# Optimization experiments

Measured on AMD Instinct MI355X. Metric: run time of the kernel, lower is better.

## Reference

```python
import jax, jax.numpy as jnp
import numpy as np

THRESHOLD = 0.3
NUM_VERTICES = 6890  # SMPL mesh
B, V, H, W = 8, 4, 512, 512


def setup_inputs() -> dict:
    key = jax.random.key(0)
    k1, k2, k3 = jax.random.split(key, 3)
    seg_maps = jax.random.uniform(k1, (B, V, H, W), dtype=jnp.float32)
    # indices in [-1, NUM_VERTICES): -1 marks background pixels (filtered as out-of-range)
    pixel_to_vertex_map = jax.random.randint(k2, (V, H, W, 3), -1, NUM_VERTICES, dtype=jnp.int32)
    bary_coord_map = jax.random.uniform(k3, (V, H, W, 3), dtype=jnp.float32)
    return {"seg_maps": seg_maps, "pixel_to_vertex_map": pixel_to_vertex_map,
            "bary_coord_map": bary_coord_map}


def reference(seg_maps, pixel_to_vertex_map, bary_coord_map):
    dtype = seg_maps.dtype
    verts = pixel_to_vertex_map                                  # [V,H,W,3]
    # a pixel contributes only if ALL 3 of its vertex ids are in range
    valid = jnp.all((verts >= 0) & (verts < NUM_VERTICES), axis=-1)  # [V,H,W]
    mask = seg_maps > THRESHOLD                                   # [B,V,H,W]
    eff = (mask & valid[None]).astype(dtype)                      # [B,V,H,W]
    w = bary_coord_map[None] * eff[..., None]                     # [B,V,H,W,3]
    ones = jnp.broadcast_to(eff[..., None], w.shape)              # per-coord count contrib
    # invalid indices were zeroed-out in weights; clamp them to 0 for a safe scatter
    idx = jnp.where(valid[..., None], verts, 0).reshape(-1)       # [V*H*W*3]
    wf = w.reshape(seg_maps.shape[0], -1)
    cf = ones.reshape(seg_maps.shape[0], -1)
    scatter = jax.vmap(lambda v: jnp.zeros((NUM_VERTICES,), dtype).at[idx].add(v))
    pred = scatter(wf)                                            # [B, NUM_VERTICES]
    count = scatter(cf)
    safe = jnp.where(count > 0, count, jnp.ones((), dtype))
    pred = jnp.where(count > 0, pred / safe, pred)
    return (pred > THRESHOLD).astype(dtype)
```

## Files before the change

kernel.cpp:

```cpp
#include <hip/hip_runtime.h>
#include <hip/hip_bf16.h>
#include <stdint.h>

#define NUM_VERTICES 6890
#define THRESHOLD 0.3f
#define B_DIM 8
#define V_DIM 4
#define H_DIM 512
#define W_DIM 512
#define TOTAL_PIX (V_DIM * H_DIM * W_DIM)
#define CHUNKS 64
#define BLOCK_THREADS 1024

#define FRAC 262144.0f
#define CNT_ONE (1u << 25)
#define SUM_MASK ((1u << 25) - 1)

__device__ __forceinline__ uint32_t pack_w(float w) {
    return CNT_ONE + (uint32_t)(w * FRAC + 0.5f);
}
__device__ __forceinline__ void lds_uadd(uint32_t* p, uint32_t v) {
    __hip_atomic_fetch_add(p, v, __ATOMIC_RELAXED, __HIP_MEMORY_SCOPE_WORKGROUP);
}

__global__ __launch_bounds__(BLOCK_THREADS)
void hc3d_accum_pair_kernel(const float* __restrict__ seg,
                            const int* __restrict__ verts,
                            const float* __restrict__ bary,
                            uint32_t* __restrict__ partial) {
    __shared__ uint32_t s_hist0[NUM_VERTICES];
    __shared__ uint32_t s_hist1[NUM_VERTICES];

    const int pr = blockIdx.y;
    const int c  = blockIdx.x;
    for (int i = threadIdx.x; i < NUM_VERTICES; i += BLOCK_THREADS) {
        s_hist0[i] = 0u;
        s_hist1[i] = 0u;
    }
    __syncthreads();

    const int groupsPerChunk = (TOTAL_PIX / CHUNKS) / 4;
    const int gStart = c * groupsPerChunk;

    const float4* __restrict__ seg0 =
        reinterpret_cast<const float4*>(seg + (size_t)(2 * pr) * TOTAL_PIX);
    const float4* __restrict__ seg1 =
        reinterpret_cast<const float4*>(seg + (size_t)(2 * pr + 1) * TOTAL_PIX);
    const int4* __restrict__ verts4  = reinterpret_cast<const int4*>(verts);
    const float4* __restrict__ bary4 = reinterpret_cast<const float4*>(bary);

    #pragma unroll 2
    for (int g = gStart + threadIdx.x; g < gStart + groupsPerChunk;
         g += BLOCK_THREADS) {
        const float4 sA = seg0[g];
        const float4 sB = seg1[g];
        const int4   va = verts4[3 * (size_t)g + 0];
        const int4   vb = verts4[3 * (size_t)g + 1];
        const int4   vc = verts4[3 * (size_t)g + 2];
        const float4 wa = bary4[3 * (size_t)g + 0];
        const float4 wb = bary4[3 * (size_t)g + 1];
        const float4 wc = bary4[3 * (size_t)g + 2];

        {
            const bool valid = ((unsigned)va.x < NUM_VERTICES) &
                               ((unsigned)va.y < NUM_VERTICES) &
                               ((unsigned)va.z < NUM_VERTICES);
            const uint32_t p0 = pack_w(wa.x), p1 = pack_w(wa.y), p2 = pack_w(wa.z);
            if (valid & (sA.x > THRESHOLD)) {
                lds_uadd(&s_hist0[va.x], p0);
                lds_uadd(&s_hist0[va.y], p1);
                lds_uadd(&s_hist0[va.z], p2);
            }
            if (valid & (sB.x > THRESHOLD)) {
                lds_uadd(&s_hist1[va.x], p0);
                lds_uadd(&s_hist1[va.y], p1);
                lds_uadd(&s_hist1[va.z], p2);
            }
        }
        {
            const bool valid = ((unsigned)va.w < NUM_VERTICES) &
                               ((unsigned)vb.x < NUM_VERTICES) &
                               ((unsigned)vb.y < NUM_VERTICES);
            const uint32_t p0 = pack_w(wa.w), p1 = pack_w(wb.x), p2 = pack_w(wb.y);
            if (valid & (sA.y > THRESHOLD)) {
                lds_uadd(&s_hist0[va.w], p0);
                lds_uadd(&s_hist0[vb.x], p1);
                lds_uadd(&s_hist0[vb.y], p2);
            }
            if (valid & (sB.y > THRESHOLD)) {
                lds_uadd(&s_hist1[va.w], p0);
                lds_uadd(&s_hist1[vb.x], p1);
                lds_uadd(&s_hist1[vb.y], p2);
            }
        }
        {
            const bool valid = ((unsigned)vb.z < NUM_VERTICES) &
                               ((unsigned)vb.w < NUM_VERTICES) &
                               ((unsigned)vc.x < NUM_VERTICES);
            const uint32_t p0 = pack_w(wb.z), p1 = pack_w(wb.w), p2 = pack_w(wc.x);
            if (valid & (sA.z > THRESHOLD)) {
                lds_uadd(&s_hist0[vb.z], p0);
                lds_uadd(&s_hist0[vb.w], p1);
                lds_uadd(&s_hist0[vc.x], p2);
            }
            if (valid & (sB.z > THRESHOLD)) {
                lds_uadd(&s_hist1[vb.z], p0);
                lds_uadd(&s_hist1[vb.w], p1);
                lds_uadd(&s_hist1[vc.x], p2);
            }
        }
        {
            const bool valid = ((unsigned)vc.y < NUM_VERTICES) &
                               ((unsigned)vc.z < NUM_VERTICES) &
                               ((unsigned)vc.w < NUM_VERTICES);
            const uint32_t p0 = pack_w(wc.y), p1 = pack_w(wc.z), p2 = pack_w(wc.w);
            if (valid & (sA.w > THRESHOLD)) {
                lds_uadd(&s_hist0[vc.y], p0);
                lds_uadd(&s_hist0[vc.z], p1);
                lds_uadd(&s_hist0[vc.w], p2);
            }
            if (valid & (sB.w > THRESHOLD)) {
                lds_uadd(&s_hist1[vc.y], p0);
                lds_uadd(&s_hist1[vc.z], p1);
                lds_uadd(&s_hist1[vc.w], p2);
            }
        }
    }
    __syncthreads();

    uint32_t* __restrict__ pb0 =
        partial + ((size_t)(c * 4 + pr) * 2 + 0) * NUM_VERTICES;
    uint32_t* __restrict__ pb1 =
        partial + ((size_t)(c * 4 + pr) * 2 + 1) * NUM_VERTICES;
    for (int i = threadIdx.x; i < NUM_VERTICES; i += BLOCK_THREADS) {
        pb0[i] = s_hist0[i];
        pb1[i] = s_hist1[i];
    }
}

__global__ __launch_bounds__(256)
void hc3d_finalize_sum_kernel(const uint32_t* __restrict__ partial,
                              float* __restrict__ out) {
    const int idx = blockIdx.x * 256 + threadIdx.x;
    if (idx < B_DIM * NUM_VERTICES) {
        const int b = idx / NUM_VERTICES;
        const int v = idx - b * NUM_VERTICES;
        const size_t slot = (size_t)b * NUM_VERTICES + v;
        uint32_t cnt = 0u, sumf = 0u;
        #pragma unroll
        for (int c = 0; c < CHUNKS; ++c) {
            const uint32_t p =
                partial[(size_t)c * (B_DIM * NUM_VERTICES) + slot];
            cnt  += p >> 25;
            sumf += p & SUM_MASK;
        }
        const float sum = (float)sumf * (1.0f / FRAC);
        const float val = (cnt > 0u) ? (sum / (float)cnt) : sum;
        out[idx] = (val > THRESHOLD) ? 1.0f : 0.0f;
    }
}

__global__ __launch_bounds__(BLOCK_THREADS)
void hc3d_accum_at_kernel(const float* __restrict__ seg,
                          const int* __restrict__ verts,
                          const float* __restrict__ bary,
                          uint32_t* __restrict__ acc) {
    const int b = blockIdx.y;
    const int c = blockIdx.x;
    const int groupsPerChunk = (TOTAL_PIX / CHUNKS) / 4;
    const int gStart = c * groupsPerChunk;
    const float4* __restrict__ seg4  =
        reinterpret_cast<const float4*>(seg + (size_t)b * TOTAL_PIX);
    const int4* __restrict__ verts4  = reinterpret_cast<const int4*>(verts);
    const float4* __restrict__ bary4 = reinterpret_cast<const float4*>(bary);
    uint32_t* predf = acc + (size_t)b * NUM_VERTICES;
    uint32_t* cnt   = acc + (size_t)(B_DIM + b) * NUM_VERTICES;

    for (int g = gStart + threadIdx.x; g < gStart + groupsPerChunk;
         g += BLOCK_THREADS) {
        const float4 s4 = seg4[g];
        const int4   va = verts4[3 * (size_t)g + 0];
        const int4   vb = verts4[3 * (size_t)g + 1];
        const int4   vc = verts4[3 * (size_t)g + 2];
        const float4 wa = bary4[3 * (size_t)g + 0];
        const float4 wb = bary4[3 * (size_t)g + 1];
        const float4 wc = bary4[3 * (size_t)g + 2];
        const float  ss[4] = {s4.x, s4.y, s4.z, s4.w};
        const int    vv[12] = {va.x,va.y,va.z, va.w,vb.x,vb.y,
                               vb.z,vb.w,vc.x, vc.y,vc.z,vc.w};
        const float  ww[12] = {wa.x,wa.y,wa.z, wa.w,wb.x,wb.y,
                               wb.z,wb.w,wc.x, wc.y,wc.z,wc.w};
        #pragma unroll
        for (int p = 0; p < 4; ++p) {
            const bool ok = (ss[p] > THRESHOLD) &
                            ((unsigned)vv[3*p+0] < NUM_VERTICES) &
                            ((unsigned)vv[3*p+1] < NUM_VERTICES) &
                            ((unsigned)vv[3*p+2] < NUM_VERTICES);
            if (ok) {
                #pragma unroll
                for (int k = 0; k < 3; ++k) {
                    atomicAdd(&predf[vv[3*p+k]],
                              (uint32_t)(ww[3*p+k] * FRAC + 0.5f));
                    atomicAdd(&cnt[vv[3*p+k]], 1u);
                }
            }
        }
    }
}

__global__ __launch_bounds__(256)
void hc3d_finalize_at_kernel(const uint32_t* __restrict__ acc,
                             float* __restrict__ out) {
    const int idx = blockIdx.x * 256 + threadIdx.x;
    if (idx < B_DIM * NUM_VERTICES) {
        const uint32_t sumf = acc[idx];
        const uint32_t cnt  = acc[(size_t)B_DIM * NUM_VERTICES + idx];
        const float sum = (float)sumf * (1.0f / FRAC);
        const float val = (cnt > 0u) ? (sum / (float)cnt) : sum;
        out[idx] = (val > THRESHOLD) ? 1.0f : 0.0f;
    }
}

extern "C" void kernel_launch(void* const* d_in, const int* in_sizes, int n_in,
                              void* d_out, int out_size, void* d_ws, size_t ws_size,
                              hipStream_t stream) {
    const float* seg   = (const float*)d_in[0];
    const int*   verts = (const int*)d_in[1];
    const float* bary  = (const float*)d_in[2];
    float* out = (float*)d_out;
    uint32_t* partial = (uint32_t*)d_ws;

    const size_t chunkBytes =
        (size_t)CHUNKS * B_DIM * NUM_VERTICES * sizeof(uint32_t);
    const int total_out = B_DIM * NUM_VERTICES;

    if (ws_size >= chunkBytes) {
        dim3 grid(CHUNKS, B_DIM / 2);
        hc3d_accum_pair_kernel<<<grid, BLOCK_THREADS, 0, stream>>>(
            seg, verts, bary, partial);
        hc3d_finalize_sum_kernel<<<(total_out + 255) / 256, 256, 0, stream>>>(
            partial, out);
    } else {
        hipMemsetAsync(partial, 0,
                       (size_t)2 * B_DIM * NUM_VERTICES * sizeof(uint32_t),
                       stream);
        dim3 grid(CHUNKS, B_DIM);
        hc3d_accum_at_kernel<<<grid, BLOCK_THREADS, 0, stream>>>(
            seg, verts, bary, partial);
        hc3d_finalize_at_kernel<<<(total_out + 255) / 256, 256, 0, stream>>>(
            partial, out);
    }
}
```

Baseline: 24.76 us.

## Process all eight batches per block with 16-bit packed dual-batch LDS histograms

Adds a kernel where each block handles one 4096-pixel tile for all eight batch items, so the vertex and barycentric maps are read once instead of four times. Batch pairs share a 32-bit LDS word through two 16-bit fields, each holding a count and a sum quantised to 1/64, which halves LDS atomics when both pixels pass the threshold. A new finalize kernel reduces 256 chunk partials. The trade-offs are coarse weight quantisation, a risk of overflowing a 16-bit field when many hits land on one vertex within a block, and the removal of the global-atomic fallback path.

```diff
diff --git a/kernel.cpp b/kernel.cpp
--- a/kernel.cpp
+++ b/kernel.cpp
@@ -9,21 +9,140 @@
 #define H_DIM 512
 #define W_DIM 512
 #define TOTAL_PIX (V_DIM * H_DIM * W_DIM)
-#define CHUNKS 64
-#define BLOCK_THREADS 1024
-
-#define FRAC 262144.0f
-#define CNT_ONE (1u << 25)
-#define SUM_MASK ((1u << 25) - 1)
-
-__device__ __forceinline__ uint32_t pack_w(float w) {
-    return CNT_ONE + (uint32_t)(w * FRAC + 0.5f);
-}
+
+#define M_CHUNKS 256
+#define M_THREADS 1024
+#define NPAIRS 4
+#define MFRAC 64.0f
+#define MCNT_ONE (1u << 11)
+#define MSUM_MASK 0x7FFu
+
 __device__ __forceinline__ void lds_uadd(uint32_t* p, uint32_t v) {
     __hip_atomic_fetch_add(p, v, __ATOMIC_RELAXED, __HIP_MEMORY_SCOPE_WORKGROUP);
 }
 
-__global__ __launch_bounds__(BLOCK_THREADS)
+__device__ __forceinline__ void do_pixel(uint32_t* s_hist,
+                                         int j0, int j1, int j2,
+                                         float w0, float w1, float w2,
+                                         float s0, float s1, float s2, float s3,
+                                         float s4, float s5, float s6, float s7) {
+    const bool valid = ((unsigned)j0 < NUM_VERTICES) &
+                       ((unsigned)j1 < NUM_VERTICES) &
+                       ((unsigned)j2 < NUM_VERTICES);
+    if (!valid) return;
+    const uint32_t pk0 = MCNT_ONE + (uint32_t)(w0 * MFRAC + 0.5f);
+    const uint32_t pk1 = MCNT_ONE + (uint32_t)(w1 * MFRAC + 0.5f);
+    const uint32_t pk2 = MCNT_ONE + (uint32_t)(w2 * MFRAC + 0.5f);
+    const uint32_t sel0 = (s0 > THRESHOLD ? 1u : 0u) | (s1 > THRESHOLD ? 0x10000u : 0u);
+    const uint32_t sel1 = (s2 > THRESHOLD ? 1u : 0u) | (s3 > THRESHOLD ? 0x10000u : 0u);
+    const uint32_t sel2 = (s4 > THRESHOLD ? 1u : 0u) | (s5 > THRESHOLD ? 0x10000u : 0u);
+    const uint32_t sel3 = (s6 > THRESHOLD ? 1u : 0u) | (s7 > THRESHOLD ? 0x10000u : 0u);
+    if (sel0) {
+        lds_uadd(&s_hist[0 * NUM_VERTICES + j0], pk0 * sel0);
+        lds_uadd(&s_hist[0 * NUM_VERTICES + j1], pk1 * sel0);
+        lds_uadd(&s_hist[0 * NUM_VERTICES + j2], pk2 * sel0);
+    }
+    if (sel1) {
+        lds_uadd(&s_hist[1 * NUM_VERTICES + j0], pk0 * sel1);
+        lds_uadd(&s_hist[1 * NUM_VERTICES + j1], pk1 * sel1);
+        lds_uadd(&s_hist[1 * NUM_VERTICES + j2], pk2 * sel1);
+    }
+    if (sel2) {
+        lds_uadd(&s_hist[2 * NUM_VERTICES + j0], pk0 * sel2);
+        lds_uadd(&s_hist[2 * NUM_VERTICES + j1], pk1 * sel2);
+        lds_uadd(&s_hist[2 * NUM_VERTICES + j2], pk2 * sel2);
+    }
+    if (sel3) {
+        lds_uadd(&s_hist[3 * NUM_VERTICES + j0], pk0 * sel3);
+        lds_uadd(&s_hist[3 * NUM_VERTICES + j1], pk1 * sel3);
+        lds_uadd(&s_hist[3 * NUM_VERTICES + j2], pk2 * sel3);
+    }
+}
+
+__global__ __launch_bounds__(M_THREADS)
+void hc3d_accum8_kernel(const float* __restrict__ seg,
+                        const int* __restrict__ verts,
+                        const float* __restrict__ bary,
+                        uint32_t* __restrict__ partial) {
+    __shared__ uint32_t s_hist[NPAIRS * NUM_VERTICES];
+
+    const int c = blockIdx.x;
+    for (int i = threadIdx.x; i < NPAIRS * NUM_VERTICES; i += M_THREADS)
+        s_hist[i] = 0u;
+    __syncthreads();
+
+    const size_t g = (size_t)c * M_THREADS + threadIdx.x;
+    const float4* __restrict__ seg4  = reinterpret_cast<const float4*>(seg);
+    const int4* __restrict__ verts4  = reinterpret_cast<const int4*>(verts);
+    const float4* __restrict__ bary4 = reinterpret_cast<const float4*>(bary);
+    const size_t SB = TOTAL_PIX / 4;
+
+    const float4 sg0 = seg4[0 * SB + g];
+    const float4 sg1 = seg4[1 * SB + g];
+    const float4 sg2 = seg4[2 * SB + g];
+    const float4 sg3 = seg4[3 * SB + g];
+    const float4 sg4 = seg4[4 * SB + g];
+    const float4 sg5 = seg4[5 * SB + g];
+    const float4 sg6 = seg4[6 * SB + g];
+    const float4 sg7 = seg4[7 * SB + g];
+    const int4   va  = verts4[3 * g + 0];
+    const int4   vb  = verts4[3 * g + 1];
+    const int4   vc  = verts4[3 * g + 2];
+    const float4 wa  = bary4[3 * g + 0];
+    const float4 wb  = bary4[3 * g + 1];
+    const float4 wc  = bary4[3 * g + 2];
+
+    do_pixel(s_hist, va.x, va.y, va.z, wa.x, wa.y, wa.z,
+             sg0.x, sg1.x, sg2.x, sg3.x, sg4.x, sg5.x, sg6.x, sg7.x);
+    do_pixel(s_hist, va.w, vb.x, vb.y, wa.w, wb.x, wb.y,
+             sg0.y, sg1.y, sg2.y, sg3.y, sg4.y, sg5.y, sg6.y, sg7.y);
+    do_pixel(s_hist, vb.z, vb.w, vc.x, wb.z, wb.w, wc.x,
+             sg0.z, sg1.z, sg2.z, sg3.z, sg4.z, sg5.z, sg6.z, sg7.z);
+    do_pixel(s_hist, vc.y, vc.z, vc.w, wc.y, wc.z, wc.w,
+             sg0.w, sg1.w, sg2.w, sg3.w, sg4.w, sg5.w, sg6.w, sg7.w);
+
+    __syncthreads();
+
+    uint32_t* __restrict__ pb = partial + (size_t)c * (NPAIRS * NUM_VERTICES);
+    for (int i = threadIdx.x; i < NPAIRS * NUM_VERTICES; i += M_THREADS)
+        pb[i] = s_hist[i];
+}
+
+__global__ __launch_bounds__(256)
+void hc3d_finalize8_kernel(const uint32_t* __restrict__ partial,
+                           float* __restrict__ out) {
+    const int t = blockIdx.x * 256 + threadIdx.x;
+    if (t < NPAIRS * NUM_VERTICES) {
+        const int q = t / NUM_VERTICES;
+        const int v = t - q * NUM_VERTICES;
+        uint32_t cntA = 0u, sumA = 0u, cntB = 0u, sumB = 0u;
+        #pragma unroll 8
+        for (int c = 0; c < M_CHUNKS; ++c) {
+            const uint32_t p =
+                partial[((size_t)c * NPAIRS + q) * NUM_VERTICES + v];
+            const uint32_t lo = p & 0xFFFFu;
+            const uint32_t hi = p >> 16;
+            cntA += lo >> 11;  sumA += lo & MSUM_MASK;
+            cntB += hi >> 11;  sumB += hi & MSUM_MASK;
+        }
+        const float mA = cntA ? ((float)sumA * (1.0f / MFRAC)) / (float)cntA : 0.0f;
+        const float mB = cntB ? ((float)sumB * (1.0f / MFRAC)) / (float)cntB : 0.0f;
+        out[(size_t)(2 * q) * NUM_VERTICES + v]     = (mA > THRESHOLD) ? 1.0f : 0.0f;
+        out[(size_t)(2 * q + 1) * NUM_VERTICES + v] = (mB > THRESHOLD) ? 1.0f : 0.0f;
+    }
+}
+
+#define P_CHUNKS 64
+#define P_THREADS 1024
+#define PFRAC 262144.0f
+#define PCNT_ONE (1u << 25)
+#define PSUM_MASK ((1u << 25) - 1)
+
+__device__ __forceinline__ uint32_t ppack_w(float w) {
+    return PCNT_ONE + (uint32_t)(w * PFRAC + 0.5f);
+}
+
+__global__ __launch_bounds__(P_THREADS)
 void hc3d_accum_pair_kernel(const float* __restrict__ seg,
                             const int* __restrict__ verts,
                             const float* __restrict__ bary,
@@ -33,15 +152,14 @@
 
     const int pr = blockIdx.y;
     const int c  = blockIdx.x;
-    for (int i = threadIdx.x; i < NUM_VERTICES; i += BLOCK_THREADS) {
+    for (int i = threadIdx.x; i < NUM_VERTICES; i += P_THREADS) {
         s_hist0[i] = 0u;
         s_hist1[i] = 0u;
     }
     __syncthreads();
 
-    const int groupsPerChunk = (TOTAL_PIX / CHUNKS) / 4;
+    const int groupsPerChunk = (TOTAL_PIX / P_CHUNKS) / 4;
     const int gStart = c * groupsPerChunk;
-
     const float4* __restrict__ seg0 =
         reinterpret_cast<const float4*>(seg + (size_t)(2 * pr) * TOTAL_PIX);
     const float4* __restrict__ seg1 =
@@ -51,7 +169,7 @@
 
     #pragma unroll 2
     for (int g = gStart + threadIdx.x; g < gStart + groupsPerChunk;
-         g += BLOCK_THREADS) {
+         g += P_THREADS) {
         const float4 sA = seg0[g];
         const float4 sB = seg1[g];
         const int4   va = verts4[3 * (size_t)g + 0];
@@ -65,7 +183,7 @@
             const bool valid = ((unsigned)va.x < NUM_VERTICES) &
                                ((unsigned)va.y < NUM_VERTICES) &
                                ((unsigned)va.z < NUM_VERTICES);
-            const uint32_t p0 = pack_w(wa.x), p1 = pack_w(wa.y), p2 = pack_w(wa.z);
+            const uint32_t p0 = ppack_w(wa.x), p1 = ppack_w(wa.y), p2 = ppack_w(wa.z);
             if (valid & (sA.x > THRESHOLD)) {
                 lds_uadd(&s_hist0[va.x], p0);
                 lds_uadd(&s_hist0[va.y], p1);
@@ -81,7 +199,7 @@
             const bool valid = ((unsigned)va.w < NUM_VERTICES) &
                                ((unsigned)vb.x < NUM_VERTICES) &
                                ((unsigned)vb.y < NUM_VERTICES);
-            const uint32_t p0 = pack_w(wa.w), p1 = pack_w(wb.x), p2 = pack_w(wb.y);
+            const uint32_t p0 = ppack_w(wa.w), p1 = ppack_w(wb.x), p2 = ppack_w(wb.y);
             if (valid & (sA.y > THRESHOLD)) {
                 lds_uadd(&s_hist0[va.w], p0);
                 lds_uadd(&s_hist0[vb.x], p1);
@@ -97,7 +215,7 @@
             const bool valid = ((unsigned)vb.z < NUM_VERTICES) &
                                ((unsigned)vb.w < NUM_VERTICES) &
                                ((unsigned)vc.x < NUM_VERTICES);
-            const uint32_t p0 = pack_w(wb.z), p1 = pack_w(wb.w), p2 = pack_w(wc.x);
+            const uint32_t p0 = ppack_w(wb.z), p1 = ppack_w(wb.w), p2 = ppack_w(wc.x);
             if (valid & (sA.z > THRESHOLD)) {
                 lds_uadd(&s_hist0[vb.z], p0);
                 lds_uadd(&s_hist0[vb.w], p1);
@@ -113,7 +231,7 @@
             const bool valid = ((unsigned)vc.y < NUM_VERTICES) &
                                ((unsigned)vc.z < NUM_VERTICES) &
                                ((unsigned)vc.w < NUM_VERTICES);
-            const uint32_t p0 = pack_w(wc.y), p1 = pack_w(wc.z), p2 = pack_w(wc.w);
+            const uint32_t p0 = ppack_w(wc.y), p1 = ppack_w(wc.z), p2 = ppack_w(wc.w);
             if (valid & (sA.w > THRESHOLD)) {
                 lds_uadd(&s_hist0[vc.y], p0);
                 lds_uadd(&s_hist0[vc.z], p1);
@@ -132,90 +250,26 @@
         partial + ((size_t)(c * 4 + pr) * 2 + 0) * NUM_VERTICES;
     uint32_t* __restrict__ pb1 =
         partial + ((size_t)(c * 4 + pr) * 2 + 1) * NUM_VERTICES;
-    for (int i = threadIdx.x; i < NUM_VERTICES; i += BLOCK_THREADS) {
+    for (int i = threadIdx.x; i < NUM_VERTICES; i += P_THREADS) {
         pb0[i] = s_hist0[i];
         pb1[i] = s_hist1[i];
     }
 }
 
 __global__ __launch_bounds__(256)
-void hc3d_finalize_sum_kernel(const uint32_t* __restrict__ partial,
-                              float* __restrict__ out) {
+void hc3d_finalize_pair_kernel(const uint32_t* __restrict__ partial,
+                               float* __restrict__ out) {
     const int idx = blockIdx.x * 256 + threadIdx.x;
     if (idx < B_DIM * NUM_VERTICES) {
-        const int b = idx / NUM_VERTICES;
-        const int v = idx - b * NUM_VERTICES;
-        const size_t slot = (size_t)b * NUM_VERTICES + v;
         uint32_t cnt = 0u, sumf = 0u;
         #pragma unroll
-        for (int c = 0; c < CHUNKS; ++c) {
+        for (int c = 0; c < P_CHUNKS; ++c) {
             const uint32_t p =
-                partial[(size_t)c * (B_DIM * NUM_VERTICES) + slot];
+                partial[(size_t)c * (B_DIM * NUM_VERTICES) + idx];
             cnt  += p >> 25;
-            sumf += p & SUM_MASK;
-        }
-        const float sum = (float)sumf * (1.0f / FRAC);
-        const float val = (cnt > 0u) ? (sum / (float)cnt) : sum;
-        out[idx] = (val > THRESHOLD) ? 1.0f : 0.0f;
-    }
-}
-
-__global__ __launch_bounds__(BLOCK_THREADS)
-void hc3d_accum_at_kernel(const float* __restrict__ seg,
-                          const int* __restrict__ verts,
-                          const float* __restrict__ bary,
-                          uint32_t* __restrict__ acc) {
-    const int b = blockIdx.y;
-    const int c = blockIdx.x;
-    const int groupsPerChunk = (TOTAL_PIX / CHUNKS) / 4;
-    const int gStart = c * groupsPerChunk;
-    const float4* __restrict__ seg4  =
-        reinterpret_cast<const float4*>(seg + (size_t)b * TOTAL_PIX);
-    const int4* __restrict__ verts4  = reinterpret_cast<const int4*>(verts);
-    const float4* __restrict__ bary4 = reinterpret_cast<const float4*>(bary);
-    uint32_t* predf = acc + (size_t)b * NUM_VERTICES;
-    uint32_t* cnt   = acc + (size_t)(B_DIM + b) * NUM_VERTICES;
-
-    for (int g = gStart + threadIdx.x; g < gStart + groupsPerChunk;
-         g += BLOCK_THREADS) {
-        const float4 s4 = seg4[g];
-        const int4   va = verts4[3 * (size_t)g + 0];
-        const int4   vb = verts4[3 * (size_t)g + 1];
-        const int4   vc = verts4[3 * (size_t)g + 2];
-        const float4 wa = bary4[3 * (size_t)g + 0];
-        const float4 wb = bary4[3 * (size_t)g + 1];
-        const float4 wc = bary4[3 * (size_t)g + 2];
-        const float  ss[4] = {s4.x, s4.y, s4.z, s4.w};
-        const int    vv[12] = {va.x,va.y,va.z, va.w,vb.x,vb.y,
-                               vb.z,vb.w,vc.x, vc.y,vc.z,vc.w};
-        const float  ww[12] = {wa.x,wa.y,wa.z, wa.w,wb.x,wb.y,
-                               wb.z,wb.w,wc.x, wc.y,wc.z,wc.w};
-        #pragma unroll
-        for (int p = 0; p < 4; ++p) {
-            const bool ok = (ss[p] > THRESHOLD) &
-                            ((unsigned)vv[3*p+0] < NUM_VERTICES) &
-                            ((unsigned)vv[3*p+1] < NUM_VERTICES) &
-                            ((unsigned)vv[3*p+2] < NUM_VERTICES);
-            if (ok) {
-                #pragma unroll
-                for (int k = 0; k < 3; ++k) {
-                    atomicAdd(&predf[vv[3*p+k]],
-                              (uint32_t)(ww[3*p+k] * FRAC + 0.5f));
-                    atomicAdd(&cnt[vv[3*p+k]], 1u);
-                }
-            }
-        }
-    }
-}
-
-__global__ __launch_bounds__(256)
-void hc3d_finalize_at_kernel(const uint32_t* __restrict__ acc,
-                             float* __restrict__ out) {
-    const int idx = blockIdx.x * 256 + threadIdx.x;
-    if (idx < B_DIM * NUM_VERTICES) {
-        const uint32_t sumf = acc[idx];
-        const uint32_t cnt  = acc[(size_t)B_DIM * NUM_VERTICES + idx];
-        const float sum = (float)sumf * (1.0f / FRAC);
+            sumf += p & PSUM_MASK;
+        }
+        const float sum = (float)sumf * (1.0f / PFRAC);
         const float val = (cnt > 0u) ? (sum / (float)cnt) : sum;
         out[idx] = (val > THRESHOLD) ? 1.0f : 0.0f;
     }
@@ -230,24 +284,23 @@
     float* out = (float*)d_out;
     uint32_t* partial = (uint32_t*)d_ws;
 
-    const size_t chunkBytes =
-        (size_t)CHUNKS * B_DIM * NUM_VERTICES * sizeof(uint32_t);
-    const int total_out = B_DIM * NUM_VERTICES;
-
-    if (ws_size >= chunkBytes) {
-        dim3 grid(CHUNKS, B_DIM / 2);
-        hc3d_accum_pair_kernel<<<grid, BLOCK_THREADS, 0, stream>>>(
+    const size_t megaBytes =
+        (size_t)M_CHUNKS * NPAIRS * NUM_VERTICES * sizeof(uint32_t);
+    const size_t pairBytes =
+        (size_t)P_CHUNKS * B_DIM * NUM_VERTICES * sizeof(uint32_t);
+
+    if (ws_size >= megaBytes) {
+        hc3d_accum8_kernel<<<M_CHUNKS, M_THREADS, 0, stream>>>(
             seg, verts, bary, partial);
-        hc3d_finalize_sum_kernel<<<(total_out + 255) / 256, 256, 0, stream>>>(
+        const int tot = NPAIRS * NUM_VERTICES;
+        hc3d_finalize8_kernel<<<(tot + 255) / 256, 256, 0, stream>>>(
             partial, out);
-    } else {
-        hipMemsetAsync(partial, 0,
-                       (size_t)2 * B_DIM * NUM_VERTICES * sizeof(uint32_t),
-                       stream);
-        dim3 grid(CHUNKS, B_DIM);
-        hc3d_accum_at_kernel<<<grid, BLOCK_THREADS, 0, stream>>>(
+    } else if (ws_size >= pairBytes) {
+        dim3 grid(P_CHUNKS, B_DIM / 2);
+        hc3d_accum_pair_kernel<<<grid, P_THREADS, 0, stream>>>(
             seg, verts, bary, partial);
-        hc3d_finalize_at_kernel<<<(total_out + 255) / 256, 256, 0, stream>>>(
+        const int tot = B_DIM * NUM_VERTICES;
+        hc3d_finalize_pair_kernel<<<(tot + 255) / 256, 256, 0, stream>>>(
             partial, out);
     }
 }
```

Measured after the change: 35.25 us. 42.4% more time.

## Prefetch first pixel group before LDS clear, fully unroll loop, parallelize finalize reduction

Applied to the files above, without the earlier changes.

The accumulate kernel now issues the global loads for its first group of pixels before zeroing the shared histograms, so the load latency overlaps the clear. The main loop becomes a fixed four-iteration unrolled loop over a shared helper. The finalize kernel now splits the 64-chunk reduction across four thread slices per vertex and combines them through shared memory, which raises parallelism in that stage. The partial layout formula is rewritten in an equivalent form, and the fully unrolled loop may raise register pressure.

```diff
diff --git a/kernel.cpp b/kernel.cpp
--- a/kernel.cpp
+++ b/kernel.cpp
@@ -9,37 +9,88 @@
 #define H_DIM 512
 #define W_DIM 512
 #define TOTAL_PIX (V_DIM * H_DIM * W_DIM)
-#define CHUNKS 64
-#define BLOCK_THREADS 1024
-
-#define FRAC 262144.0f
-#define CNT_ONE (1u << 25)
-#define SUM_MASK ((1u << 25) - 1)
-
-__device__ __forceinline__ uint32_t pack_w(float w) {
-    return CNT_ONE + (uint32_t)(w * FRAC + 0.5f);
-}
+
+#define P_CHUNKS 64
+#define P_THREADS 1024
+#define PFRAC 262144.0f
+#define PCNT_ONE (1u << 25)
+#define PSUM_MASK ((1u << 25) - 1)
+
 __device__ __forceinline__ void lds_uadd(uint32_t* p, uint32_t v) {
     __hip_atomic_fetch_add(p, v, __ATOMIC_RELAXED, __HIP_MEMORY_SCOPE_WORKGROUP);
 }
-
-__global__ __launch_bounds__(BLOCK_THREADS)
+__device__ __forceinline__ uint32_t ppack_w(float w) {
+    return PCNT_ONE + (uint32_t)(w * PFRAC + 0.5f);
+}
+
+__device__ __forceinline__ void pair_group(uint32_t* __restrict__ h0,
+                                           uint32_t* __restrict__ h1,
+                                           const float4& sA, const float4& sB,
+                                           const int4& va, const int4& vb,
+                                           const int4& vc,
+                                           const float4& wa, const float4& wb,
+                                           const float4& wc) {
+    {
+        const bool valid = ((unsigned)va.x < NUM_VERTICES) &
+                           ((unsigned)va.y < NUM_VERTICES) &
+                           ((unsigned)va.z < NUM_VERTICES);
+        const uint32_t p0 = ppack_w(wa.x), p1 = ppack_w(wa.y), p2 = ppack_w(wa.z);
+        if (valid & (sA.x > THRESHOLD)) {
+            lds_uadd(&h0[va.x], p0); lds_uadd(&h0[va.y], p1); lds_uadd(&h0[va.z], p2);
+        }
+        if (valid & (sB.x > THRESHOLD)) {
+            lds_uadd(&h1[va.x], p0); lds_uadd(&h1[va.y], p1); lds_uadd(&h1[va.z], p2);
+        }
+    }
+    {
+        const bool valid = ((unsigned)va.w < NUM_VERTICES) &
+                           ((unsigned)vb.x < NUM_VERTICES) &
+                           ((unsigned)vb.y < NUM_VERTICES);
+        const uint32_t p0 = ppack_w(wa.w), p1 = ppack_w(wb.x), p2 = ppack_w(wb.y);
+        if (valid & (sA.y > THRESHOLD)) {
+            lds_uadd(&h0[va.w], p0); lds_uadd(&h0[vb.x], p1); lds_uadd(&h0[vb.y], p2);
+        }
+        if (valid & (sB.y > THRESHOLD)) {
+            lds_uadd(&h1[va.w], p0); lds_uadd(&h1[vb.x], p1); lds_uadd(&h1[vb.y], p2);
+        }
+    }
+    {
+        const bool valid = ((unsigned)vb.z < NUM_VERTICES) &
+                           ((unsigned)vb.w < NUM_VERTICES) &
+                           ((unsigned)vc.x < NUM_VERTICES);
+        const uint32_t p0 = ppack_w(wb.z), p1 = ppack_w(wb.w), p2 = ppack_w(wc.x);
+        if (valid & (sA.z > THRESHOLD)) {
+            lds_uadd(&h0[vb.z], p0); lds_uadd(&h0[vb.w], p1); lds_uadd(&h0[vc.x], p2);
+        }
+        if (valid & (sB.z > THRESHOLD)) {
+            lds_uadd(&h1[vb.z], p0); lds_uadd(&h1[vb.w], p1); lds_uadd(&h1[vc.x], p2);
+        }
+    }
+    {
+        const bool valid = ((unsigned)vc.y < NUM_VERTICES) &
+                           ((unsigned)vc.z < NUM_VERTICES) &
+                           ((unsigned)vc.w < NUM_VERTICES);
+        const uint32_t p0 = ppack_w(wc.y), p1 = ppack_w(wc.z), p2 = ppack_w(wc.w);
+        if (valid & (sA.w > THRESHOLD)) {
+            lds_uadd(&h0[vc.y], p0); lds_uadd(&h0[vc.z], p1); lds_uadd(&h0[vc.w], p2);
+        }
+        if (valid & (sB.w > THRESHOLD)) {
+            lds_uadd(&h1[vc.y], p0); lds_uadd(&h1[vc.z], p1); lds_uadd(&h1[vc.w], p2);
+        }
+    }
+}
+
+__global__ __launch_bounds__(P_THREADS)
 void hc3d_accum_pair_kernel(const float* __restrict__ seg,
                             const int* __restrict__ verts,
                             const float* __restrict__ bary,
                             uint32_t* __restrict__ partial) {
-    __shared__ uint32_t s_hist0[NUM_VERTICES];
-    __shared__ uint32_t s_hist1[NUM_VERTICES];
+    __shared__ uint32_t h0[NUM_VERTICES];
+    __shared__ uint32_t h1[NUM_VERTICES];
 
     const int pr = blockIdx.y;
     const int c  = blockIdx.x;
-    for (int i = threadIdx.x; i < NUM_VERTICES; i += BLOCK_THREADS) {
-        s_hist0[i] = 0u;
-        s_hist1[i] = 0u;
-    }
-    __syncthreads();
-
-    const int groupsPerChunk = (TOTAL_PIX / CHUNKS) / 4;
+    const int groupsPerChunk = (TOTAL_PIX / P_CHUNKS) / 4;
     const int gStart = c * groupsPerChunk;
 
     const float4* __restrict__ seg0 =
@@ -49,125 +100,94 @@
     const int4* __restrict__ verts4  = reinterpret_cast<const int4*>(verts);
     const float4* __restrict__ bary4 = reinterpret_cast<const float4*>(bary);
 
-    #pragma unroll 2
-    for (int g = gStart + threadIdx.x; g < gStart + groupsPerChunk;
-         g += BLOCK_THREADS) {
+    const size_t g0 = (size_t)gStart + threadIdx.x;
+    const float4 sA_0 = seg0[g0];
+    const float4 sB_0 = seg1[g0];
+    const int4   va_0 = verts4[3 * g0 + 0];
+    const int4   vb_0 = verts4[3 * g0 + 1];
+    const int4   vc_0 = verts4[3 * g0 + 2];
+    const float4 wa_0 = bary4[3 * g0 + 0];
+    const float4 wb_0 = bary4[3 * g0 + 1];
+    const float4 wc_0 = bary4[3 * g0 + 2];
+
+    for (int i = threadIdx.x; i < NUM_VERTICES; i += P_THREADS) {
+        h0[i] = 0u;
+        h1[i] = 0u;
+    }
+    __syncthreads();
+
+    pair_group(h0, h1, sA_0, sB_0, va_0, vb_0, vc_0, wa_0, wb_0, wc_0);
+
+    #pragma unroll
+    for (int it = 1; it < 4; ++it) {
+        const size_t g = (size_t)gStart + (size_t)it * P_THREADS + threadIdx.x;
         const float4 sA = seg0[g];
         const float4 sB = seg1[g];
-        const int4   va = verts4[3 * (size_t)g + 0];
-        const int4   vb = verts4[3 * (size_t)g + 1];
-        const int4   vc = verts4[3 * (size_t)g + 2];
-        const float4 wa = bary4[3 * (size_t)g + 0];
-        const float4 wb = bary4[3 * (size_t)g + 1];
-        const float4 wc = bary4[3 * (size_t)g + 2];
-
-        {
-            const bool valid = ((unsigned)va.x < NUM_VERTICES) &
-                               ((unsigned)va.y < NUM_VERTICES) &
-                               ((unsigned)va.z < NUM_VERTICES);
-            const uint32_t p0 = pack_w(wa.x), p1 = pack_w(wa.y), p2 = pack_w(wa.z);
-            if (valid & (sA.x > THRESHOLD)) {
-                lds_uadd(&s_hist0[va.x], p0);
-                lds_uadd(&s_hist0[va.y], p1);
-                lds_uadd(&s_hist0[va.z], p2);
-            }
-            if (valid & (sB.x > THRESHOLD)) {
-                lds_uadd(&s_hist1[va.x], p0);
-                lds_uadd(&s_hist1[va.y], p1);
-                lds_uadd(&s_hist1[va.z], p2);
-            }
-        }
-        {
-            const bool valid = ((unsigned)va.w < NUM_VERTICES) &
-                               ((unsigned)vb.x < NUM_VERTICES) &
-                               ((unsigned)vb.y < NUM_VERTICES);
-            const uint32_t p0 = pack_w(wa.w), p1 = pack_w(wb.x), p2 = pack_w(wb.y);
-            if (valid & (sA.y > THRESHOLD)) {
-                lds_uadd(&s_hist0[va.w], p0);
-                lds_uadd(&s_hist0[vb.x], p1);
-                lds_uadd(&s_hist0[vb.y], p2);
-            }
-            if (valid & (sB.y > THRESHOLD)) {
-                lds_uadd(&s_hist1[va.w], p0);
-                lds_uadd(&s_hist1[vb.x], p1);
-                lds_uadd(&s_hist1[vb.y], p2);
-            }
-        }
-        {
-            const bool valid = ((unsigned)vb.z < NUM_VERTICES) &
-                               ((unsigned)vb.w < NUM_VERTICES) &
-                               ((unsigned)vc.x < NUM_VERTICES);
-            const uint32_t p0 = pack_w(wb.z), p1 = pack_w(wb.w), p2 = pack_w(wc.x);
-            if (valid & (sA.z > THRESHOLD)) {
-                lds_uadd(&s_hist0[vb.z], p0);
-                lds_uadd(&s_hist0[vb.w], p1);
-                lds_uadd(&s_hist0[vc.x], p2);
-            }
-            if (valid & (sB.z > THRESHOLD)) {
-                lds_uadd(&s_hist1[vb.z], p0);
-                lds_uadd(&s_hist1[vb.w], p1);
-                lds_uadd(&s_hist1[vc.x], p2);
-            }
-        }
-        {
-            const bool valid = ((unsigned)vc.y < NUM_VERTICES) &
-                               ((unsigned)vc.z < NUM_VERTICES) &
-                               ((unsigned)vc.w < NUM_VERTICES);
-            const uint32_t p0 = pack_w(wc.y), p1 = pack_w(wc.z), p2 = pack_w(wc.w);
-            if (valid & (sA.w > THRESHOLD)) {
-                lds_uadd(&s_hist0[vc.y], p0);
-                lds_uadd(&s_hist0[vc.z], p1);
-                lds_uadd(&s_hist0[vc.w], p2);
-            }
-            if (valid & (sB.w > THRESHOLD)) {
-                lds_uadd(&s_hist1[vc.y], p0);
-                lds_uadd(&s_hist1[vc.z], p1);
-                lds_uadd(&s_hist1[vc.w], p2);
-            }
-        }
+        const int4   va = verts4[3 * g + 0];
+        const int4   vb = verts4[3 * g + 1];
+        const int4   vc = verts4[3 * g + 2];
+        const float4 wa = bary4[3 * g + 0];
+        const float4 wb = bary4[3 * g + 1];
+        const float4 wc = bary4[3 * g + 2];
+        pair_group(h0, h1, sA, sB, va, vb, vc, wa, wb, wc);
     }
     __syncthreads();
 
     uint32_t* __restrict__ pb0 =
-        partial + ((size_t)(c * 4 + pr) * 2 + 0) * NUM_VERTICES;
+        partial + ((size_t)c * 8 + 2 * pr + 0) * NUM_VERTICES;
     uint32_t* __restrict__ pb1 =
-        partial + ((size_t)(c * 4 + pr) * 2 + 1) * NUM_VERTICES;
-    for (int i = threadIdx.x; i < NUM_VERTICES; i += BLOCK_THREADS) {
-        pb0[i] = s_hist0[i];
-        pb1[i] = s_hist1[i];
-    }
-}
-
-__global__ __launch_bounds__(256)
-void hc3d_finalize_sum_kernel(const uint32_t* __restrict__ partial,
+        partial + ((size_t)c * 8 + 2 * pr + 1) * NUM_VERTICES;
+    for (int i = threadIdx.x; i < NUM_VERTICES; i += P_THREADS) {
+        pb0[i] = h0[i];
+        pb1[i] = h1[i];
+    }
+}
+
+__global__ __launch_bounds__(1024)
+void hc3d_finalize_par_kernel(const uint32_t* __restrict__ partial,
                               float* __restrict__ out) {
-    const int idx = blockIdx.x * 256 + threadIdx.x;
-    if (idx < B_DIM * NUM_VERTICES) {
-        const int b = idx / NUM_VERTICES;
-        const int v = idx - b * NUM_VERTICES;
-        const size_t slot = (size_t)b * NUM_VERTICES + v;
-        uint32_t cnt = 0u, sumf = 0u;
+    __shared__ uint32_t scnt[4][256];
+    __shared__ uint32_t ssum[4][256];
+
+    const int b  = blockIdx.y;
+    const int vt = blockIdx.x;
+    const int vl = threadIdx.x & 255;
+    const int s  = threadIdx.x >> 8;
+    const int v  = vt * 256 + vl;
+
+    uint32_t cnt = 0u, sumf = 0u;
+    if (v < NUM_VERTICES) {
+        for (int c = s; c < P_CHUNKS; c += 4) {
+            const uint32_t p = partial[((size_t)c * 8 + b) * NUM_VERTICES + v];
+            cnt  += p >> 25;
+            sumf += p & PSUM_MASK;
+        }
+    }
+    scnt[s][vl] = cnt;
+    ssum[s][vl] = sumf;
+    __syncthreads();
+
+    if (s == 0 && v < NUM_VERTICES) {
+        uint32_t C = 0u, S = 0u;
         #pragma unroll
-        for (int c = 0; c < CHUNKS; ++c) {
-            const uint32_t p =
-                partial[(size_t)c * (B_DIM * NUM_VERTICES) + slot];
-            cnt  += p >> 25;
-            sumf += p & SUM_MASK;
-        }
-        const float sum = (float)sumf * (1.0f / FRAC);
-        const float val = (cnt > 0u) ? (sum / (float)cnt) : sum;
-        out[idx] = (val > THRESHOLD) ? 1.0f : 0.0f;
-    }
-}
-
-__global__ __launch_bounds__(BLOCK_THREADS)
+        for (int k = 0; k < 4; ++k) {
+            C += scnt[k][vl];
+            S += ssum[k][vl];
+        }
+        const float sum = (float)S * (1.0f / PFRAC);
+        const float val = C ? (sum / (float)C) : sum;
+        out[(size_t)b * NUM_VERTICES + v] = (val > THRESHOLD) ? 1.0f : 0.0f;
+    }
+}
+
+__global__ __launch_bounds__(1024)
 void hc3d_accum_at_kernel(const float* __restrict__ seg,
                           const int* __restrict__ verts,
                           const float* __restrict__ bary,
                           uint32_t* __restrict__ acc) {
     const int b = blockIdx.y;
     const int c = blockIdx.x;
-    const int groupsPerChunk = (TOTAL_PIX / CHUNKS) / 4;
+    const int groupsPerChunk = (TOTAL_PIX / 64) / 4;
     const int gStart = c * groupsPerChunk;
     const float4* __restrict__ seg4  =
         reinterpret_cast<const float4*>(seg + (size_t)b * TOTAL_PIX);
@@ -176,8 +196,8 @@
     uint32_t* predf = acc + (size_t)b * NUM_VERTICES;
     uint32_t* cnt   = acc + (size_t)(B_DIM + b) * NUM_VERTICES;
 
-    for (int g = gStart + threadIdx.x; g < gStart + groupsPerChunk;
-         g += BLOCK_THREADS) {
+    for (int g = gStart + (int)threadIdx.x; g < gStart + groupsPerChunk;
+         g += 1024) {
         const float4 s4 = seg4[g];
         const int4   va = verts4[3 * (size_t)g + 0];
         const int4   vb = verts4[3 * (size_t)g + 1];
@@ -200,7 +220,7 @@
                 #pragma unroll
                 for (int k = 0; k < 3; ++k) {
                     atomicAdd(&predf[vv[3*p+k]],
-                              (uint32_t)(ww[3*p+k] * FRAC + 0.5f));
+                              (uint32_t)(ww[3*p+k] * PFRAC + 0.5f));
                     atomicAdd(&cnt[vv[3*p+k]], 1u);
                 }
             }
@@ -215,7 +235,7 @@
     if (idx < B_DIM * NUM_VERTICES) {
         const uint32_t sumf = acc[idx];
         const uint32_t cnt  = acc[(size_t)B_DIM * NUM_VERTICES + idx];
-        const float sum = (float)sumf * (1.0f / FRAC);
+        const float sum = (float)sumf * (1.0f / PFRAC);
         const float val = (cnt > 0u) ? (sum / (float)cnt) : sum;
         out[idx] = (val > THRESHOLD) ? 1.0f : 0.0f;
     }
@@ -230,24 +250,24 @@
     float* out = (float*)d_out;
     uint32_t* partial = (uint32_t*)d_ws;
 
-    const size_t chunkBytes =
-        (size_t)CHUNKS * B_DIM * NUM_VERTICES * sizeof(uint32_t);
-    const int total_out = B_DIM * NUM_VERTICES;
-
-    if (ws_size >= chunkBytes) {
-        dim3 grid(CHUNKS, B_DIM / 2);
-        hc3d_accum_pair_kernel<<<grid, BLOCK_THREADS, 0, stream>>>(
+    const size_t pairBytes =
+        (size_t)P_CHUNKS * B_DIM * NUM_VERTICES * sizeof(uint32_t);
+
+    if (ws_size >= pairBytes) {
+        dim3 agrid(P_CHUNKS, B_DIM / 2);
+        hc3d_accum_pair_kernel<<<agrid, P_THREADS, 0, stream>>>(
             seg, verts, bary, partial);
-        hc3d_finalize_sum_kernel<<<(total_out + 255) / 256, 256, 0, stream>>>(
-            partial, out);
+        dim3 fgrid((NUM_VERTICES + 255) / 256, B_DIM);
+        hc3d_finalize_par_kernel<<<fgrid, 1024, 0, stream>>>(partial, out);
     } else {
         hipMemsetAsync(partial, 0,
                        (size_t)2 * B_DIM * NUM_VERTICES * sizeof(uint32_t),
                        stream);
-        dim3 grid(CHUNKS, B_DIM);
-        hc3d_accum_at_kernel<<<grid, BLOCK_THREADS, 0, stream>>>(
+        dim3 grid(64, B_DIM);
+        hc3d_accum_at_kernel<<<grid, 1024, 0, stream>>>(
             seg, verts, bary, partial);
-        hc3d_finalize_at_kernel<<<(total_out + 255) / 256, 256, 0, stream>>>(
+        const int tot = B_DIM * NUM_VERTICES;
+        hc3d_finalize_at_kernel<<<(tot + 255) / 256, 256, 0, stream>>>(
             partial, out);
     }
 }
```

New measurement: 23.55 us. -4.9%, faster.
